# Kernel optimization log

Measured on AMD Instinct MI355X. Metric: run time of the kernel, lower is better.

## Reference

```python
import jax, jax.numpy as jnp
import numpy as np


def setup_inputs() -> dict:
    key = jax.random.key(0)
    k1, k2, k3 = jax.random.split(key, 3)
    B, C_in, H, W = 16, 256, 64, 64
    C_out, KH, KW = 256, 3, 3
    x = jax.random.normal(k1, (B, C_in, H, W), dtype=jnp.float32)
    # kaiming-uniform-like scale for realism
    fan_in = C_in * KH * KW
    bound = 1.0 / np.sqrt(fan_in)
    weights = jax.random.normal(k2, (C_out, C_in, KH, KW), dtype=jnp.float32) * bound
    bias = jax.random.uniform(k3, (C_out,), dtype=jnp.float32, minval=-bound, maxval=bound)
    return {"x": x, "weights": weights, "bias": bias}


def reference(x, weights, bias):
    # Conv2dApproximation with approximation_enable=False is an exact conv2d:
    # input is unfolded to [B, C*kh*kw, oh, ow], weights to [C_out, C*kh*kw],
    # and the MultiApp kernel performs the exact MAC (see exact matmul backward).
    # stride=(1,1), padding=(0,0), dilation=(1,1) per init_kwargs.
    out = jax.lax.conv_general_dilated(
        x, weights,
        window_strides=(1, 1),
        padding=((0, 0), (0, 0)),
        rhs_dilation=(1, 1),
        dimension_numbers=("NCHW", "OIHW", "NCHW"),
    )
    return out + bias[None, :, None, None]
```

## Files before the change

kernel.cpp:

```cpp
#include <hip/hip_runtime.h>
#include <stdint.h>

typedef short short8 __attribute__((ext_vector_type(8)));
typedef float f32x4 __attribute__((ext_vector_type(4)));

#define AS1 __attribute__((address_space(1)))
#define AS3 __attribute__((address_space(3)))

__device__ __forceinline__ void gl_lds16(const void* g, void* l) {
  __builtin_amdgcn_global_load_lds((const AS1 unsigned int*)g,
                                   (AS3 unsigned int*)l, 16, 0, 0);
}

__device__ __forceinline__ unsigned short f2bf(float f) {
  union { float f; unsigned int u; } v; v.f = f;
  return (unsigned short)((v.u + (((v.u >> 16) & 1u) + 0x7fffu)) >> 16);
}

__global__ __launch_bounds__(256) void xpose_kernel(const float* __restrict__ x,
                                                    unsigned short* __restrict__ xt) {
  __shared__ float tile[64][68];
  const int bid = blockIdx.x;
  const int cchunk = bid & 3;
  const int y = (bid >> 2) & 63;
  const int b = bid >> 8;
  const int t = threadIdx.x;
  const int ci0 = cchunk * 64;

  const int cc = t >> 2;
  const int xo = (t & 3) * 16;
  const float* src = x + (((size_t)(b * 256 + ci0 + cc) * 64 + y) * 64 + xo);
  float4 v0 = ((const float4*)src)[0];
  float4 v1 = ((const float4*)src)[1];
  float4 v2 = ((const float4*)src)[2];
  float4 v3 = ((const float4*)src)[3];
  *(float4*)&tile[cc][xo + 0]  = v0;
  *(float4*)&tile[cc][xo + 4]  = v1;
  *(float4*)&tile[cc][xo + 8]  = v2;
  *(float4*)&tile[cc][xo + 12] = v3;
  __syncthreads();

  const int xpos = t >> 2;
  const int ccg = (t & 3) * 16;
  unsigned int pk[8];
#pragma unroll
  for (int e = 0; e < 8; ++e) {
    unsigned int lo = f2bf(tile[ccg + 2 * e][xpos]);
    unsigned int hi = f2bf(tile[ccg + 2 * e + 1][xpos]);
    pk[e] = lo | (hi << 16);
  }
  unsigned short* dst = xt + ((size_t)(b * 4096 + y * 64 + xpos) * 256 + ci0 + ccg);
  uint4 w0; w0.x = pk[0]; w0.y = pk[1]; w0.z = pk[2]; w0.w = pk[3];
  uint4 w1; w1.x = pk[4]; w1.y = pk[5]; w1.z = pk[6]; w1.w = pk[7];
  ((uint4*)dst)[0] = w0;
  ((uint4*)dst)[1] = w1;
}

__global__ __launch_bounds__(256) void wpack_kernel(const float* __restrict__ w,
                                                    unsigned short* __restrict__ wrp) {
  const int idx = blockIdx.x * 256 + threadIdx.x;
  const int ci = idx & 255;
  const int co = (idx >> 8) & 255;
  const int p = idx >> 16;
  wrp[idx] = f2bf(w[(size_t)(co * 256 + ci) * 9 + p]);
}

__global__ __launch_bounds__(512, 2) void conv_ring4(
    const unsigned short* __restrict__ xt,
    const unsigned short* __restrict__ wrp,
    const float* __restrict__ bias,
    float* __restrict__ out) {
  __shared__ unsigned short lds[4][16384];

  const int tid = threadIdx.x;
  const int lane = tid & 63;
  const int wv = tid >> 6;
  const int wm = wv >> 2;
  const int wn = wv & 3;
  const int bid = blockIdx.x;
  const int tile = (bid & 7) * 32 + (bid >> 3);
  const int b = tile >> 4;
  const int oh0 = (tile & 15) * 4;

  const int srow = tid >> 2;
  const int slin = tid & 3;
  const int sw = slin ^ (srow & 3);
  const unsigned short* gA = wrp + (size_t)srow * 256 + sw * 8;
  const unsigned short* gB[2];
#pragma unroll
  for (int i = 0; i < 2; ++i) {
    const int px = i * 128 + srow;
    const int y = min(oh0 + (px >> 6), 61);
    const int xc = min(px & 63, 61);
    gB[i] = xt + ((size_t)(b * 64 + y) * 64 + xc) * 256 + sw * 8;
  }
  const unsigned dstA = srow * 32 + slin * 8;

  auto stageA = [&](int kt2) {
    const int tap = kt2 >> 3, ci0 = (kt2 & 7) * 32;
    unsigned short* s = &lds[kt2 & 3][0];
    const unsigned short* g = gA + tap * 65536 + ci0;
    gl_lds16(g, s + dstA);
    gl_lds16(g + 128 * 256, s + 4096 + dstA);
  };
  auto stageB = [&](int kt2) {
    const int tap = kt2 >> 3, ci0 = (kt2 & 7) * 32;
    const int kh = (tap * 11) >> 5, kw = tap - kh * 3;
    const int off = (kh * 64 + kw) * 256 + ci0;
    unsigned short* s = &lds[kt2 & 3][0];
    gl_lds16(gB[0] + off, s + 8192 + dstA);
    gl_lds16(gB[1] + off, s + 8192 + 4096 + dstA);
  };

  const int l15 = lane & 15;
  const int fsl = (((lane >> 4)) ^ (l15 & 3)) * 8;

  f32x4 acc[8][4] = {};

  stageA(0); stageB(0);
  stageA(1); stageB(1);
  asm volatile("s_waitcnt vmcnt(4)" ::: "memory");
  __builtin_amdgcn_s_barrier();

  for (int kt = 0; kt < 72; ++kt) {
    const unsigned short* s = &lds[kt & 3][0];
    short8 af[4], bf[4];

#pragma unroll
    for (int m = 0; m < 4; ++m)
      af[m] = *(const short8*)(s + (wm * 128 + m * 16 + l15) * 32 + fsl);
#pragma unroll
    for (int n = 0; n < 4; ++n)
      bf[n] = *(const short8*)(s + 8192 + (wn * 64 + n * 16 + l15) * 32 + fsl);
    if (kt < 70) stageA(kt + 2);
    __builtin_amdgcn_s_barrier();
    __builtin_amdgcn_s_setprio(1);
#pragma unroll
    for (int m = 0; m < 4; ++m)
#pragma unroll
      for (int n = 0; n < 4; ++n)
        acc[m][n] = __builtin_amdgcn_mfma_f32_16x16x32_bf16(af[m], bf[n], acc[m][n], 0, 0, 0);
    __builtin_amdgcn_s_setprio(0);
    asm volatile("s_waitcnt lgkmcnt(0)" ::: "memory");
    __builtin_amdgcn_s_barrier();

#pragma unroll
    for (int m = 0; m < 4; ++m)
      af[m] = *(const short8*)(s + (wm * 128 + (4 + m) * 16 + l15) * 32 + fsl);
    if (kt < 70) stageB(kt + 2);
    __builtin_amdgcn_s_barrier();
    __builtin_amdgcn_s_setprio(1);
#pragma unroll
    for (int m = 0; m < 4; ++m)
#pragma unroll
      for (int n = 0; n < 4; ++n)
        acc[4 + m][n] = __builtin_amdgcn_mfma_f32_16x16x32_bf16(af[m], bf[n], acc[4 + m][n], 0, 0, 0);
    __builtin_amdgcn_s_setprio(0);
    asm volatile("s_waitcnt lgkmcnt(0)" ::: "memory");
    if (kt <= 69)      asm volatile("s_waitcnt vmcnt(4)" ::: "memory");
    else if (kt == 70) asm volatile("s_waitcnt vmcnt(0)" ::: "memory");
    __builtin_amdgcn_s_barrier();
  }

  const int rb = (lane >> 4) * 4;
  const int colp = lane & 15;
#pragma unroll
  for (int m = 0; m < 8; ++m) {
    const int co = wm * 128 + m * 16 + rb;
    float bv[4];
#pragma unroll
    for (int j = 0; j < 4; ++j) bv[j] = bias[co + j];
#pragma unroll
    for (int n = 0; n < 4; ++n) {
      const int px = wn * 64 + n * 16 + colp;
      const int prow = px >> 6, ow = px & 63;
      const int oh = oh0 + prow;
      if (ow < 62 && oh < 62) {
#pragma unroll
        for (int j = 0; j < 4; ++j)
          out[((size_t)(b * 256 + co + j) * 62 + oh) * 62 + ow] = acc[m][n][j] + bv[j];
      }
    }
  }
}

__global__ __launch_bounds__(256) void conv_naive(const float* __restrict__ x,
                                                  const float* __restrict__ wgt,
                                                  const float* __restrict__ bias,
                                                  float* __restrict__ out) {
  const size_t idx = (size_t)blockIdx.x * 256 + threadIdx.x;
  if (idx >= (size_t)16 * 256 * 62 * 62) return;
  const int ow = (int)(idx % 62);
  size_t r = idx / 62;
  const int oh = (int)(r % 62); r /= 62;
  const int co = (int)(r % 256);
  const int b = (int)(r / 256);
  float s = bias[co];
  for (int ci = 0; ci < 256; ++ci) {
    const float* xp = x + ((size_t)(b * 256 + ci) * 64 + oh) * 64 + ow;
    const float* wp = wgt + (size_t)(co * 256 + ci) * 9;
#pragma unroll
    for (int kh = 0; kh < 3; ++kh)
#pragma unroll
      for (int kw = 0; kw < 3; ++kw)
        s += xp[kh * 64 + kw] * wp[kh * 3 + kw];
  }
  out[idx] = s;
}

extern "C" void kernel_launch(void* const* d_in, const int* in_sizes, int n_in,
                              void* d_out, int out_size, void* d_ws, size_t ws_size,
                              hipStream_t stream) {
  const float* x = (const float*)d_in[0];
  const float* wgt = (const float*)d_in[1];
  const float* bias = (const float*)d_in[2];
  float* out = (float*)d_out;

  const size_t xt_elems = (size_t)16 * 64 * 64 * 256;
  const size_t wr_elems = (size_t)9 * 256 * 256;
  const size_t need = (xt_elems + wr_elems) * sizeof(unsigned short);

  if (ws_size < need) {
    conv_naive<<<61504, 256, 0, stream>>>(x, wgt, bias, out);
    return;
  }

  unsigned short* xt = (unsigned short*)d_ws;
  unsigned short* wrp = xt + xt_elems;

  xpose_kernel<<<4096, 256, 0, stream>>>(x, xt);
  wpack_kernel<<<2304, 256, 0, stream>>>(wgt, wrp);
  conv_ring4<<<256, 512, 0, stream>>>(xt, wrp, bias, out);
}
```

Before: 104.7 us.

## Deepen LDS ring prefetch and double-buffer fragment registers across k-tiles

```diff
diff --git a/kernel.cpp b/kernel.cpp
--- a/kernel.cpp
+++ b/kernel.cpp
@@ -65,7 +65,7 @@
   wrp[idx] = f2bf(w[(size_t)(co * 256 + ci) * 9 + p]);
 }
 
-__global__ __launch_bounds__(512, 2) void conv_ring4(
+__global__ __launch_bounds__(512, 2) void conv_r4p(
     const unsigned short* __restrict__ xt,
     const unsigned short* __restrict__ wrp,
     const float* __restrict__ bias,
@@ -84,7 +84,7 @@
 
   const int srow = tid >> 2;
   const int slin = tid & 3;
-  const int sw = slin ^ (srow & 3);
+  const int sw = slin ^ ((srow >> 1) & 3);
   const unsigned short* gA = wrp + (size_t)srow * 256 + sw * 8;
   const unsigned short* gB[2];
 #pragma unroll
@@ -98,75 +98,97 @@
 
   auto stageA = [&](int kt2) {
     const int tap = kt2 >> 3, ci0 = (kt2 & 7) * 32;
-    unsigned short* s = &lds[kt2 & 3][0];
+    unsigned short* sl = &lds[kt2 & 3][0];
     const unsigned short* g = gA + tap * 65536 + ci0;
-    gl_lds16(g, s + dstA);
-    gl_lds16(g + 128 * 256, s + 4096 + dstA);
+    gl_lds16(g, sl + dstA);
+    gl_lds16(g + 128 * 256, sl + 4096 + dstA);
   };
   auto stageB = [&](int kt2) {
     const int tap = kt2 >> 3, ci0 = (kt2 & 7) * 32;
     const int kh = (tap * 11) >> 5, kw = tap - kh * 3;
     const int off = (kh * 64 + kw) * 256 + ci0;
-    unsigned short* s = &lds[kt2 & 3][0];
-    gl_lds16(gB[0] + off, s + 8192 + dstA);
-    gl_lds16(gB[1] + off, s + 8192 + 4096 + dstA);
+    unsigned short* sl = &lds[kt2 & 3][0];
+    gl_lds16(gB[0] + off, sl + 8192 + dstA);
+    gl_lds16(gB[1] + off, sl + 8192 + 4096 + dstA);
   };
 
   const int l15 = lane & 15;
-  const int fsl = (((lane >> 4)) ^ (l15 & 3)) * 8;
+  const int fsl = ((lane >> 4) ^ ((l15 >> 1) & 3)) * 8;
+  int aoff[8], boff[4];
+#pragma unroll
+  for (int a = 0; a < 8; ++a)
+    aoff[a] = (wm * 128 + (a >> 2) * 64 + (a & 3) * 16 + l15) * 32 + fsl;
+#pragma unroll
+  for (int n = 0; n < 4; ++n)
+    boff[n] = 8192 + (wn * 64 + n * 16 + l15) * 32 + fsl;
 
   f32x4 acc[8][4] = {};
 
   stageA(0); stageB(0);
   stageA(1); stageB(1);
+  stageA(2); stageB(2);
   asm volatile("s_waitcnt vmcnt(4)" ::: "memory");
   __builtin_amdgcn_s_barrier();
 
-  for (int kt = 0; kt < 72; ++kt) {
-    const unsigned short* s = &lds[kt & 3][0];
-    short8 af[4], bf[4];
-
-#pragma unroll
-    for (int m = 0; m < 4; ++m)
-      af[m] = *(const short8*)(s + (wm * 128 + m * 16 + l15) * 32 + fsl);
-#pragma unroll
-    for (int n = 0; n < 4; ++n)
-      bf[n] = *(const short8*)(s + 8192 + (wn * 64 + n * 16 + l15) * 32 + fsl);
-    if (kt < 70) stageA(kt + 2);
-    __builtin_amdgcn_s_barrier();
-    __builtin_amdgcn_s_setprio(1);
-#pragma unroll
-    for (int m = 0; m < 4; ++m)
-#pragma unroll
-      for (int n = 0; n < 4; ++n)
-        acc[m][n] = __builtin_amdgcn_mfma_f32_16x16x32_bf16(af[m], bf[n], acc[m][n], 0, 0, 0);
-    __builtin_amdgcn_s_setprio(0);
-    asm volatile("s_waitcnt lgkmcnt(0)" ::: "memory");
-    __builtin_amdgcn_s_barrier();
-
-#pragma unroll
-    for (int m = 0; m < 4; ++m)
-      af[m] = *(const short8*)(s + (wm * 128 + (4 + m) * 16 + l15) * 32 + fsl);
-    if (kt < 70) stageB(kt + 2);
-    __builtin_amdgcn_s_barrier();
-    __builtin_amdgcn_s_setprio(1);
-#pragma unroll
-    for (int m = 0; m < 4; ++m)
-#pragma unroll
-      for (int n = 0; n < 4; ++n)
-        acc[4 + m][n] = __builtin_amdgcn_mfma_f32_16x16x32_bf16(af[m], bf[n], acc[4 + m][n], 0, 0, 0);
-    __builtin_amdgcn_s_setprio(0);
-    asm volatile("s_waitcnt lgkmcnt(0)" ::: "memory");
-    if (kt <= 69)      asm volatile("s_waitcnt vmcnt(4)" ::: "memory");
-    else if (kt == 70) asm volatile("s_waitcnt vmcnt(0)" ::: "memory");
-    __builtin_amdgcn_s_barrier();
-  }
+  short8 aC0[4], bC0[4], aC1[4], bC1[4], a2[4];
+  {
+    const unsigned short* s0 = &lds[0][0];
+#pragma unroll
+    for (int q = 0; q < 4; ++q) aC0[q] = *(const short8*)(s0 + aoff[q]);
+#pragma unroll
+    for (int n = 0; n < 4; ++n) bC0[n] = *(const short8*)(s0 + boff[n]);
+  }
+
+#define KTILE(KT, AC, BC, ANX, BNX)                                            \
+  {                                                                            \
+    const int kt_ = (KT);                                                      \
+    const unsigned short* s_ = &lds[kt_ & 3][0];                               \
+    const unsigned short* sn_ = &lds[(kt_ + 1) & 3][0];                        \
+    _Pragma("unroll")                                                          \
+    for (int q = 0; q < 4; ++q) a2[q] = *(const short8*)(s_ + aoff[4 + q]);    \
+    if (kt_ < 69) stageA(kt_ + 3);                                             \
+    __builtin_amdgcn_sched_barrier(0);                                         \
+    __builtin_amdgcn_s_setprio(1);                                             \
+    _Pragma("unroll")                                                          \
+    for (int q = 0; q < 4; ++q)                                                \
+      _Pragma("unroll")                                                        \
+      for (int n = 0; n < 4; ++n)                                              \
+        acc[q][n] = __builtin_amdgcn_mfma_f32_16x16x32_bf16(AC[q], BC[n],      \
+                                                            acc[q][n], 0, 0, 0); \
+    __builtin_amdgcn_s_setprio(0);                                             \
+    if (kt_ < 71) {                                                            \
+      _Pragma("unroll")                                                        \
+      for (int q = 0; q < 4; ++q) ANX[q] = *(const short8*)(sn_ + aoff[q]);    \
+      _Pragma("unroll")                                                        \
+      for (int n = 0; n < 4; ++n) BNX[n] = *(const short8*)(sn_ + boff[n]);    \
+    }                                                                          \
+    if (kt_ < 69) stageB(kt_ + 3);                                             \
+    __builtin_amdgcn_sched_barrier(0);                                         \
+    __builtin_amdgcn_s_setprio(1);                                             \
+    _Pragma("unroll")                                                          \
+    for (int q = 0; q < 4; ++q)                                                \
+      _Pragma("unroll")                                                        \
+      for (int n = 0; n < 4; ++n)                                              \
+        acc[4 + q][n] = __builtin_amdgcn_mfma_f32_16x16x32_bf16(a2[q], BC[n],  \
+                                                                acc[4 + q][n], 0, 0, 0); \
+    __builtin_amdgcn_s_setprio(0);                                             \
+    asm volatile("s_waitcnt lgkmcnt(8)" ::: "memory");                         \
+    if (kt_ < 69)       asm volatile("s_waitcnt vmcnt(4)" ::: "memory");       \
+    else if (kt_ == 69) asm volatile("s_waitcnt vmcnt(0)" ::: "memory");       \
+    __builtin_amdgcn_s_barrier();                                              \
+  }
+
+  for (int it = 0; it < 36; ++it) {
+    KTILE(2 * it,     aC0, bC0, aC1, bC1);
+    KTILE(2 * it + 1, aC1, bC1, aC0, bC0);
+  }
+#undef KTILE
 
   const int rb = (lane >> 4) * 4;
   const int colp = lane & 15;
 #pragma unroll
-  for (int m = 0; m < 8; ++m) {
-    const int co = wm * 128 + m * 16 + rb;
+  for (int a = 0; a < 8; ++a) {
+    const int co = wm * 128 + (a >> 2) * 64 + (a & 3) * 16 + rb;
     float bv[4];
 #pragma unroll
     for (int j = 0; j < 4; ++j) bv[j] = bias[co + j];
@@ -178,7 +200,7 @@
       if (ow < 62 && oh < 62) {
 #pragma unroll
         for (int j = 0; j < 4; ++j)
-          out[((size_t)(b * 256 + co + j) * 62 + oh) * 62 + ow] = acc[m][n][j] + bv[j];
+          out[((size_t)(b * 256 + co + j) * 62 + oh) * 62 + ow] = acc[a][n][j] + bv[j];
       }
     }
   }
@@ -230,5 +252,5 @@
 
   xpose_kernel<<<4096, 256, 0, stream>>>(x, xt);
   wpack_kernel<<<2304, 256, 0, stream>>>(wgt, wrp);
-  conv_ring4<<<256, 512, 0, stream>>>(xt, wrp, bias, out);
-}
+  conv_r4p<<<256, 512, 0, stream>>>(xt, wrp, bias, out);
+}
```

After: 96.02 us. 8.3% less time.
